# Performance work log

Measured on AMD Instinct MI355X. Metric: run time of the kernel, lower is better.

## Reference

```python
import jax, jax.numpy as jnp
import numpy as np

D_MODEL = 768
NUM_HEADS = 12
D_K = D_MODEL // NUM_HEADS
B, S = 2, 2048


def setup_inputs() -> dict:
    key = jax.random.key(0)
    ks = jax.random.split(key, 7)
    scale = 1.0 / np.sqrt(D_MODEL)
    return {
        "query": jax.random.normal(ks[0], (B, S, D_MODEL), jnp.float32),
        "key_in": jax.random.normal(ks[1], (B, S, D_MODEL), jnp.float32),
        "value": jax.random.normal(ks[2], (B, S, D_MODEL), jnp.float32),
        # nn.Linear weights are [out, in]; y = x @ W.T
        "Wq": jax.random.normal(ks[3], (D_MODEL, D_MODEL), jnp.float32) * scale,
        "Wk": jax.random.normal(ks[4], (D_MODEL, D_MODEL), jnp.float32) * scale,
        "Wv": jax.random.normal(ks[5], (D_MODEL, D_MODEL), jnp.float32) * scale,
        "Wo": jax.random.normal(ks[6], (D_MODEL, D_MODEL), jnp.float32) * scale,
    }


def _split_heads(x):
    b, s, _ = x.shape
    return x.reshape(b, s, NUM_HEADS, D_K).transpose(0, 2, 1, 3)  # [B,H,S,Dk]


def reference(query, key_in, value, Wq, Wk, Wv, Wo):
    Q = _split_heads(query @ Wq.T)
    K = _split_heads(key_in @ Wk.T)
    V = _split_heads(value @ Wv.T)
    scores = jnp.einsum("bhqd,bhkd->bhqk", Q, K) / jnp.sqrt(jnp.float32(D_K))
    attn = jax.nn.softmax(scores, axis=-1)
    ctx = jnp.einsum("bhqk,bhkd->bhqd", attn, V)  # [B,H,S,Dk]
    ctx = ctx.transpose(0, 2, 1, 3).reshape(query.shape[0], query.shape[1], D_MODEL)
    return ctx @ Wo.T
```

## Files before the change

kernel.cpp:

```cpp
#include <hip/hip_runtime.h>
#include <hip/hip_bf16.h>


typedef __bf16 bf16x8 __attribute__((ext_vector_type(8)));
typedef float f32x4 __attribute__((ext_vector_type(4)));
typedef unsigned short u16;
typedef unsigned int u32;
typedef u16 u16x8 __attribute__((ext_vector_type(8)));
typedef u16 u16x4 __attribute__((ext_vector_type(4)));

#define SEQ 2048
#define DM  768
#define NH  12
#define DK  64
#define NBH 24
#define MTOT 4096
#define NEL 3145728
#define NWL 589824

__device__ __forceinline__ u16 f2b(float v) {
  __bf16 t = (__bf16)v;
  return __builtin_bit_cast(u16, t);
}

__device__ __forceinline__ void gl_lds16(const u16* g, u16* l) {
  __builtin_amdgcn_global_load_lds(
      (const __attribute__((address_space(1))) void*)g,
      (__attribute__((address_space(3))) void*)l, 16, 0, 0);
}

__device__ __forceinline__ int pos32(int k) {
  return (k < 16) ? (((k >> 2) << 3) + (k & 3))
                  : ((((k & 15) >> 2) << 3) + (k & 3) + 4);
}


__global__ __launch_bounds__(256) void to_bf16(
    const float* __restrict__ s0, const float* __restrict__ s1, const float* __restrict__ s2,
    const float* __restrict__ s3, const float* __restrict__ s4, const float* __restrict__ s5,
    const float* __restrict__ s6, u16* __restrict__ Xb, u16* __restrict__ Wb)
{
  size_t c = (size_t)blockIdx.x * 256 + threadIdx.x;
  const float* src;
  u16* dst;
  if (c < 1179648) {
    int seg = (int)(c / 393216);
    size_t off = (c % 393216) * 8;
    src = (seg == 0 ? s0 : seg == 1 ? s1 : s2) + off;
    dst = Xb + (size_t)seg * NEL + off;
  } else {
    size_t c2 = c - 1179648;
    int seg = (int)(c2 / 73728);
    size_t off = (c2 % 73728) * 8;
    src = (seg == 0 ? s3 : seg == 1 ? s4 : seg == 2 ? s5 : s6) + off;
    dst = Wb + (size_t)seg * NWL + off;
  }
  float4 f0 = *(const float4*)(src);
  float4 f1 = *(const float4*)(src + 4);
  u16x8 o;
  o[0] = f2b(f0.x); o[1] = f2b(f0.y); o[2] = f2b(f0.z); o[3] = f2b(f0.w);
  o[4] = f2b(f1.x); o[5] = f2b(f1.y); o[6] = f2b(f1.z); o[7] = f2b(f1.w);
  *(u16x8*)dst = o;
}

__device__ __forceinline__ void gemm2_core(
    const u16* __restrict__ X, const u16* __restrict__ W, void* __restrict__ Y,
    int m0, int n0, int mode, u16* As, u16* Bs)
{
  const int tid  = threadIdx.x;
  const int lane = tid & 63, w = tid >> 6;
  const int l15  = lane & 15, quad = lane >> 4;
  const int wm   = (w & 1) * 64, wn = (w >> 1) * 64;

  f32x4 acc[4][4] = {};

  for (int k0 = 0; k0 < DM; k0 += 64) {
    __syncthreads();
#pragma unroll
    for (int i = 0; i < 4; i++) {
      int c = (w * 4 + i) * 64 + lane;
      int row = c >> 3, c8 = c & 7;
      int g8 = c8 ^ (row & 7);
      gl_lds16(X + (size_t)(m0 + row) * DM + k0 + g8 * 8, As + c * 8);
      gl_lds16(W + (size_t)(n0 + row) * DM + k0 + g8 * 8, Bs + c * 8);
    }
    __syncthreads();
#pragma unroll
    for (int dk = 0; dk < 2; dk++) {
      bf16x8 af[4], bf[4];
      int ph = ((dk * 4 + quad) ^ (l15 & 7)) * 8;
#pragma unroll
      for (int t = 0; t < 4; t++) {
        af[t] = *(const bf16x8*)(&As[(wm + t * 16 + l15) * 64 + ph]);
        bf[t] = *(const bf16x8*)(&Bs[(wn + t * 16 + l15) * 64 + ph]);
      }
#pragma unroll
      for (int mt = 0; mt < 4; mt++)
#pragma unroll
        for (int nt = 0; nt < 4; nt++)
          acc[mt][nt] = __builtin_amdgcn_mfma_f32_16x16x32_bf16(af[mt], bf[nt], acc[mt][nt], 0, 0, 0);
    }
  }

  if (mode == 2) {
    float* O = (float*)Y;
#pragma unroll
    for (int mt = 0; mt < 4; mt++) {
      int mg = m0 + wm + mt * 16 + quad * 4;
#pragma unroll
      for (int nt = 0; nt < 4; nt++) {
        int j = n0 + wn + nt * 16 + l15;
#pragma unroll
        for (int r = 0; r < 4; r++)
          O[(size_t)(mg + r) * DM + j] = acc[mt][nt][r];
      }
    }
  } else if (mode == 1) {
    u16* O = (u16*)Y;
#pragma unroll
    for (int mt = 0; mt < 4; mt++) {
      int mg = m0 + wm + mt * 16 + quad * 4;
      int b = mg >> 11, s = mg & 2047;
      int sp = (s & ~31) | pos32(s & 31);
#pragma unroll
      for (int nt = 0; nt < 4; nt++) {
        int j = n0 + wn + nt * 16 + l15;
        int h = j >> 6, d = j & 63;
        u16x4 o;
#pragma unroll
        for (int r = 0; r < 4; r++) o[r] = f2b(acc[mt][nt][r]);
        *(u16x4*)&O[((size_t)(b * NH + h) * DK + d) * SEQ + sp] = o;
      }
    }
  } else {
    u16* O = (u16*)Y;
    u16* T = As;
#pragma unroll
    for (int h2 = 0; h2 < 2; h2++) {
      __syncthreads();
      if ((w & 1) == h2) {
#pragma unroll
        for (int mt = 0; mt < 4; mt++)
#pragma unroll
          for (int nt = 0; nt < 4; nt++)
#pragma unroll
            for (int r = 0; r < 4; r++)
              T[(mt * 16 + quad * 4 + r) * 128 + wn + nt * 16 + l15] = f2b(acc[mt][nt][r]);
      }
      __syncthreads();
#pragma unroll
      for (int i = 0; i < 4; i++) {
        int c = i * 256 + tid;
        int row = c >> 4, ch = c & 15;
        u16x8 val = *(const u16x8*)&T[row * 128 + ch * 8];
        int m = m0 + h2 * 64 + row;
        int j = n0 + ch * 8;
        int hh = j >> 6, d = j & 63;
        int b = m >> 11, s = m & 2047;
        *(u16x8*)&O[((size_t)(b * NH + hh) * SEQ + s) * DK + d] = val;
      }
    }
  }
}

__global__ __launch_bounds__(256) void qkv2(
    const u16* __restrict__ Xb, const u16* __restrict__ Wb,
    u16* __restrict__ Qhm, u16* __restrict__ Khm, u16* __restrict__ Vt)
{
  __shared__ __align__(16) u16 As[128 * 64];
  __shared__ __align__(16) u16 Bs[128 * 64];
  int mat = blockIdx.z;
  const u16* X = Xb + (size_t)mat * NEL;
  const u16* W = Wb + (size_t)mat * NWL;
  void* Y = (mat == 0) ? (void*)Qhm : (mat == 1) ? (void*)Khm : (void*)Vt;
  gemm2_core(X, W, Y, blockIdx.y * 128, blockIdx.x * 128, (mat == 2) ? 1 : 0, As, Bs);
}

__global__ __launch_bounds__(256) void bt2(
    const u16* __restrict__ Ctx, const u16* __restrict__ Wob, float* __restrict__ Y)
{
  __shared__ __align__(16) u16 As[128 * 64];
  __shared__ __align__(16) u16 Bs[128 * 64];
  gemm2_core(Ctx, Wob, Y, blockIdx.y * 128, blockIdx.x * 128, 2, As, Bs);
}

__global__ __launch_bounds__(256) void attn2(
    const u16* __restrict__ Qh, const u16* __restrict__ Kh,
    const u16* __restrict__ Vt, u16* __restrict__ ctx)
{
  __shared__ __align__(16) u16 smem[128 * 64 + 64 * 128];
  __shared__ float Ls[64];
  u16* Ks = smem;
  u16* Vs = smem + 128 * 64;

  const int tid  = threadIdx.x;
  const int lane = tid & 63, w = tid >> 6;
  const int l15  = lane & 15, quad = lane >> 4;
  const int qh = w & 1, kh = w >> 1;
  const int qt = blockIdx.x, bh = blockIdx.y;
  const int b = bh / NH, h = bh % NH;

  const u16* Qb = Qh + (size_t)bh * SEQ * DK;
  const u16* Kb = Kh + (size_t)bh * SEQ * DK;
  const u16* Vb = Vt + (size_t)bh * DK * SEQ;
  const int q0 = qt * 64 + qh * 32;

  bf16x8 qf[2][2];
#pragma unroll
  for (int QT = 0; QT < 2; QT++)
#pragma unroll
    for (int dk = 0; dk < 2; dk++)
      qf[QT][dk] = *(const bf16x8*)&Qb[(size_t)(q0 + QT * 16 + l15) * DK + dk * 32 + quad * 8];

  float lpart[2] = {0.f, 0.f};
  f32x4 oacc[4][2] = {};

  for (int kt = 0; kt < SEQ; kt += 128) {
    __syncthreads();
#pragma unroll
    for (int i = 0; i < 4; i++) {
      int c = (w * 4 + i) * 64 + lane;
      int row = c >> 3, c8 = c & 7;
      gl_lds16(Kb + (size_t)(kt + row) * DK + (c8 ^ (row & 7)) * 8, Ks + c * 8);
    }
#pragma unroll
    for (int i = 0; i < 4; i++) {
      int c = (w * 4 + i) * 64 + lane;
      int d = c >> 4, c16 = c & 15;
      gl_lds16(Vb + (size_t)d * SEQ + kt + (c16 ^ (d & 15)) * 8, Vs + c * 8);
    }
    __syncthreads();

    f32x4 sc[4][2] = {};
#pragma unroll
    for (int MT = 0; MT < 4; MT++) {
      int row = kh * 64 + MT * 16 + l15;
#pragma unroll
      for (int dk = 0; dk < 2; dk++) {
        bf16x8 kf = *(const bf16x8*)&Ks[row * 64 + ((dk * 4 + quad) ^ (l15 & 7)) * 8];
        sc[MT][0] = __builtin_amdgcn_mfma_f32_16x16x32_bf16(kf, qf[0][dk], sc[MT][0], 0, 0, 0);
        sc[MT][1] = __builtin_amdgcn_mfma_f32_16x16x32_bf16(kf, qf[1][dk], sc[MT][1], 0, 0, 0);
      }
    }

    bf16x8 pf[2][2];
#pragma unroll
    for (int QT = 0; QT < 2; QT++)
#pragma unroll
      for (int kk = 0; kk < 2; kk++)
#pragma unroll
        for (int j = 0; j < 8; j++) {
          float s = sc[kk * 2 + (j >> 2)][QT][j & 3] * 0.125f;
          float p = __expf(fminf(s, 30.0f));
          lpart[QT] += p;
          pf[kk][QT][j] = (__bf16)p;
        }

#pragma unroll
    for (int kk = 0; kk < 2; kk++) {
      int cL = kh * 8 + kk * 4 + quad;
#pragma unroll
      for (int DT = 0; DT < 4; DT++) {
        int d = DT * 16 + l15;
        bf16x8 vf = *(const bf16x8*)&Vs[d * 128 + (cL ^ (d & 15)) * 8];
        oacc[DT][0] = __builtin_amdgcn_mfma_f32_16x16x32_bf16(vf, pf[kk][0], oacc[DT][0], 0, 0, 0);
        oacc[DT][1] = __builtin_amdgcn_mfma_f32_16x16x32_bf16(vf, pf[kk][1], oacc[DT][1], 0, 0, 0);
      }
    }
  }

  __syncthreads();

  float lw[2];
#pragma unroll
  for (int QT = 0; QT < 2; QT++) {
    float l = lpart[QT];
    l += __shfl_xor(l, 16);
    l += __shfl_xor(l, 32);
    lw[QT] = l;
  }

  float* Os = (float*)smem;
  float* Ob = Os + qh * (32 * 68);
  if (kh == 1) {
#pragma unroll
    for (int DT = 0; DT < 4; DT++)
#pragma unroll
      for (int QT = 0; QT < 2; QT++)
        *(f32x4*)&Ob[(QT * 16 + l15) * 68 + DT * 16 + quad * 4] = oacc[DT][QT];
    if (quad == 0) {
      Ls[qh * 32 + l15]      = lw[0];
      Ls[qh * 32 + 16 + l15] = lw[1];
    }
  }
  __syncthreads();
  if (kh == 0) {
#pragma unroll
    for (int QT = 0; QT < 2; QT++) {
      float inv = 1.0f / (lw[QT] + Ls[qh * 32 + QT * 16 + l15]);
      int s = q0 + QT * 16 + l15;
#pragma unroll
      for (int DT = 0; DT < 4; DT++) {
        f32x4 add = *(const f32x4*)&Ob[(QT * 16 + l15) * 68 + DT * 16 + quad * 4];
        u16x4 ov;
#pragma unroll
        for (int r = 0; r < 4; r++)
          ov[r] = f2b((oacc[DT][QT][r] + add[r]) * inv);
        *(u16x4*)&ctx[((size_t)(b * SEQ + s)) * DM + h * DK + DT * 16 + quad * 4] = ov;
      }
    }
  }
}


__device__ __forceinline__ void stage8(u16* dst, const void* src, size_t elemIdx, int isf32) {
  if (isf32) {
    const float* s = (const float*)src + elemIdx;
    float4 f0 = *(const float4*)(s);
    float4 f1 = *(const float4*)(s + 4);
    u16x8 o;
    o[0] = f2b(f0.x); o[1] = f2b(f0.y); o[2] = f2b(f0.z); o[3] = f2b(f0.w);
    o[4] = f2b(f1.x); o[5] = f2b(f1.y); o[6] = f2b(f1.z); o[7] = f2b(f1.w);
    *(u16x8*)dst = o;
  } else {
    *(float4*)dst = *(const float4*)((const u16*)src + elemIdx);
  }
}

__device__ __forceinline__ void gemm_core_fb(
    const void* __restrict__ X, const void* __restrict__ W, void* __restrict__ Y,
    int m0, int n0, int out_mode, u16* As, u16* Bs, int xf32, int wf32)
{
  const int tid  = threadIdx.x;
  const int lane = tid & 63, w = tid >> 6;
  const int l15  = lane & 15, quad = lane >> 4;
  const int wm   = (w & 1) * 64, wn = (w >> 1) * 64;
  f32x4 acc[4][4] = {};
  for (int k0 = 0; k0 < DM; k0 += 32) {
    __syncthreads();
#pragma unroll
    for (int i = 0; i < 2; i++) {
      int c = i * 256 + tid;
      int row = c >> 2, cc = c & 3;
      stage8(&As[c * 8], X, (size_t)(m0 + row) * DM + k0 + cc * 8, xf32);
      stage8(&Bs[c * 8], W, (size_t)(n0 + row) * DM + k0 + cc * 8, wf32);
    }
    __syncthreads();
    bf16x8 af[4], bf[4];
#pragma unroll
    for (int t = 0; t < 4; t++) {
      af[t] = *(const bf16x8*)(&As[(wm + t * 16 + l15) * 32 + quad * 8]);
      bf[t] = *(const bf16x8*)(&Bs[(wn + t * 16 + l15) * 32 + quad * 8]);
    }
#pragma unroll
    for (int mt = 0; mt < 4; mt++)
#pragma unroll
      for (int nt = 0; nt < 4; nt++)
        acc[mt][nt] = __builtin_amdgcn_mfma_f32_16x16x32_bf16(af[mt], bf[nt], acc[mt][nt], 0, 0, 0);
  }
  if (out_mode == 2) {
    float* O = (float*)Y;
#pragma unroll
    for (int mt = 0; mt < 4; mt++) {
      int mg = m0 + wm + mt * 16 + quad * 4;
#pragma unroll
      for (int nt = 0; nt < 4; nt++) {
        int j = n0 + wn + nt * 16 + l15;
#pragma unroll
        for (int r = 0; r < 4; r++)
          O[(size_t)(mg + r) * DM + j] = acc[mt][nt][r];
      }
    }
  } else {
    u16* O = (u16*)Y;
#pragma unroll
    for (int mt = 0; mt < 4; mt++) {
      int mg = m0 + wm + mt * 16 + quad * 4;
#pragma unroll
      for (int nt = 0; nt < 4; nt++) {
        int j = n0 + wn + nt * 16 + l15;
        int h = j >> 6, d = j & 63;
#pragma unroll
        for (int r = 0; r < 4; r++) {
          int m = mg + r;
          int b = m >> 11, s = m & 2047;
          O[((size_t)(b * NH + h) * SEQ + s) * DK + d] = f2b(acc[mt][nt][r]);
        }
      }
    }
  }
}

__global__ __launch_bounds__(256) void fb_qkv_gemm(
    const float* __restrict__ Xq, const float* __restrict__ Xk, const float* __restrict__ Xv,
    const float* __restrict__ Wq, const float* __restrict__ Wk, const float* __restrict__ Wv,
    u16* __restrict__ Yq, u16* __restrict__ Yk, u16* __restrict__ Yv)
{
  __shared__ __align__(16) u16 As[128 * 32];
  __shared__ __align__(16) u16 Bs[128 * 32];
  int mat = blockIdx.z;
  const float* X = (mat == 0) ? Xq : (mat == 1) ? Xk : Xv;
  const float* W = (mat == 0) ? Wq : (mat == 1) ? Wk : Wv;
  u16*         Y = (mat == 0) ? Yq : (mat == 1) ? Yk : Yv;
  gemm_core_fb(X, W, Y, blockIdx.y * 128, blockIdx.x * 128, 0, As, Bs, 1, 1);
}

__global__ __launch_bounds__(256) void fb_gemm_bt(
    const u16* __restrict__ X, const float* __restrict__ W, float* __restrict__ Y)
{
  __shared__ __align__(16) u16 As[128 * 32];
  __shared__ __align__(16) u16 Bs[128 * 32];
  gemm_core_fb(X, W, Y, blockIdx.y * 128, blockIdx.x * 128, 2, As, Bs, 0, 1);
}

__global__ __launch_bounds__(256) void fb_attn(
    const u16* __restrict__ Qh, const u16* __restrict__ Kh,
    const u16* __restrict__ Vh, u16* __restrict__ ctx)
{
  __shared__ __align__(16) u16 Ks[32 * 88];
  __shared__ __align__(16) u16 Vs[64 * 40];
  __shared__ __align__(16) u16 Ps[4][16 * 32];
  const int tid  = threadIdx.x;
  const int lane = tid & 63, w = tid >> 6;
  const int l15  = lane & 15, quad = lane >> 4;
  const int qt = blockIdx.x, bh = blockIdx.y;
  const int b = bh / NH, h = bh % NH;
  const u16* Qb = Qh + (size_t)bh * SEQ * DK;
  const u16* Kb = Kh + (size_t)bh * SEQ * DK;
  const u16* Vb = Vh + (size_t)bh * SEQ * DK;
  const int q0 = qt * 64 + w * 16;
  bf16x8 qf[2];
#pragma unroll
  for (int kk = 0; kk < 2; kk++)
    qf[kk] = *(const bf16x8*)(&Qb[(size_t)(q0 + l15) * DK + kk * 32 + quad * 8]);
  float m_i[4] = {-INFINITY, -INFINITY, -INFINITY, -INFINITY};
  float l_i[4] = {0.f, 0.f, 0.f, 0.f};
  f32x4 acc[4] = {};
  for (int kt = 0; kt < SEQ; kt += 32) {
    __syncthreads();
    {
      int c = tid;
      int row = c >> 3, c8 = c & 7;
      *(float4*)(&Ks[row * 88 + c8 * 8]) =
          *(const float4*)(&Kb[(size_t)(kt + row) * DK + c8 * 8]);
    }
#pragma unroll
    for (int i = 0; i < 4; i++) {
      int e = i * 256 + tid;
      int k = e >> 5, d2 = e & 31;
      u32 v = *(const u32*)(&Vb[(size_t)(kt + k) * DK + d2 * 2]);
      Vs[(d2 * 2)     * 40 + k] = (u16)(v & 0xffffu);
      Vs[(d2 * 2 + 1) * 40 + k] = (u16)(v >> 16);
    }
    __syncthreads();
    f32x4 sc[2] = {};
#pragma unroll
    for (int ktt = 0; ktt < 2; ktt++)
#pragma unroll
      for (int dk = 0; dk < 2; dk++) {
        bf16x8 kf = *(const bf16x8*)(&Ks[(ktt * 16 + l15) * 88 + dk * 32 + quad * 8]);
        sc[ktt] = __builtin_amdgcn_mfma_f32_16x16x32_bf16(qf[dk], kf, sc[ktt], 0, 0, 0);
      }
    float alph[4];
#pragma unroll
    for (int r = 0; r < 4; r++) {
      float s0 = sc[0][r] * 0.125f;
      float s1 = sc[1][r] * 0.125f;
      float mv = fmaxf(s0, s1);
      mv = fmaxf(mv, __shfl_xor(mv, 1));
      mv = fmaxf(mv, __shfl_xor(mv, 2));
      mv = fmaxf(mv, __shfl_xor(mv, 4));
      mv = fmaxf(mv, __shfl_xor(mv, 8));
      float mnew = fmaxf(m_i[r], mv);
      float a = __expf(m_i[r] - mnew);
      m_i[r] = mnew;
      float p0 = __expf(s0 - mnew);
      float p1 = __expf(s1 - mnew);
      float rs = p0 + p1;
      rs += __shfl_xor(rs, 1);
      rs += __shfl_xor(rs, 2);
      rs += __shfl_xor(rs, 4);
      rs += __shfl_xor(rs, 8);
      l_i[r] = l_i[r] * a + rs;
      alph[r] = a;
      Ps[w][(quad * 4 + r) * 32 +      l15] = f2b(p0);
      Ps[w][(quad * 4 + r) * 32 + 16 + l15] = f2b(p1);
    }
#pragma unroll
    for (int nt = 0; nt < 4; nt++) {
      acc[nt][0] *= alph[0];
      acc[nt][1] *= alph[1];
      acc[nt][2] *= alph[2];
      acc[nt][3] *= alph[3];
    }
    __syncthreads();
    bf16x8 pf = *(const bf16x8*)(&Ps[w][l15 * 32 + quad * 8]);
#pragma unroll
    for (int nt = 0; nt < 4; nt++) {
      bf16x8 vf = *(const bf16x8*)(&Vs[(nt * 16 + l15) * 40 + quad * 8]);
      acc[nt] = __builtin_amdgcn_mfma_f32_16x16x32_bf16(pf, vf, acc[nt], 0, 0, 0);
    }
  }
#pragma unroll
  for (int nt = 0; nt < 4; nt++) {
    int d = nt * 16 + l15;
#pragma unroll
    for (int r = 0; r < 4; r++) {
      int s = q0 + quad * 4 + r;
      float v = acc[nt][r] / l_i[r];
      ctx[((size_t)(b * SEQ + s)) * DM + h * DK + d] = f2b(v);
    }
  }
}


extern "C" void kernel_launch(void* const* d_in, const int* in_sizes, int n_in,
                              void* d_out, int out_size, void* d_ws, size_t ws_size,
                              hipStream_t stream) {
  const float* act[3] = {nullptr, nullptr, nullptr};
  const float* wgt[4] = {nullptr, nullptr, nullptr, nullptr};
  int na = 0, nw = 0;
  for (int i = 0; i < n_in && i < 7; i++) {
    if (in_sizes[i] == NEL) { if (na < 3) act[na++] = (const float*)d_in[i]; }
    else                    { if (nw < 4) wgt[nw++] = (const float*)d_in[i]; }
  }
  const float* q  = act[0] ? act[0] : (const float*)d_in[0];
  const float* k  = act[1] ? act[1] : (const float*)d_in[1];
  const float* v  = act[2] ? act[2] : (const float*)d_in[2];
  const float* Wq = wgt[0] ? wgt[0] : (const float*)d_in[3];
  const float* Wk = wgt[1] ? wgt[1] : (const float*)d_in[4];
  const float* Wv = wgt[2] ? wgt[2] : (const float*)d_in[5];
  const float* Wo = wgt[3] ? wgt[3] : (const float*)d_in[6];
  u16* ws = (u16*)d_ws;

  const size_t NE = NEL, NW = NWL;
  const size_t need = (6 * NE + 4 * NW) * 2;

  if (ws_size >= need) {
    u16* Xb  = ws;
    u16* Wb  = ws + 3 * NE;
    u16* Qhm = Wb + 4 * NW;
    u16* Khm = Qhm + NE;
    u16* Vt  = Khm + NE;
    u16* Ctx = ws;

    to_bf16<<<5760, 256, 0, stream>>>(q, k, v, Wq, Wk, Wv, Wo, Xb, Wb);
    qkv2<<<dim3(DM / 128, MTOT / 128, 3), 256, 0, stream>>>(Xb, Wb, Qhm, Khm, Vt);
    attn2<<<dim3(SEQ / 64, NBH), 256, 0, stream>>>(Qhm, Khm, Vt, Ctx);
    bt2<<<dim3(DM / 128, MTOT / 128), 256, 0, stream>>>(Ctx, Wb + 3 * NW, (float*)d_out);
  } else {
    u16* Qhm = ws;
    u16* Khm = ws + NE;
    u16* Vhm = ws + 2 * NE;
    u16* Ctx = ws + 3 * NE;
    fb_qkv_gemm<<<dim3(DM / 128, MTOT / 128, 3), 256, 0, stream>>>(
        q, k, v, Wq, Wk, Wv, Qhm, Khm, Vhm);
    fb_attn<<<dim3(SEQ / 64, NBH), 256, 0, stream>>>(Qhm, Khm, Vhm, Ctx);
    fb_gemm_bt<<<dim3(DM / 128, MTOT / 128), 256, 0, stream>>>(Ctx, Wo, (float*)d_out);
  }
}
```

Measured before the change: 194.2 us.

## Double-buffer GEMM and attention tiles, remap blocks per XCD, fold softmax scale

The projection and output GEMMs, and the attention kernel, now double-buffer their LDS tiles so the next global-to-LDS load is issued while the current tile is being computed. Blocks are mapped onto a 1D grid with an XCD-aware ordering, and launch bounds request two blocks per CU. The softmax scale (1/sqrt(d_k) * log2 e) is folded into the Q projection, so attention can use exp2 directly. Row sums are accumulated with an MFMA against a vector of ones, and each wave now covers 32 queries across all keys, which removes the cross-wave LDS reduction at the end. The trade-offs are twice the LDS per block and the loss of the score clamp, which raises overflow risk for large logits.

After: 166.3 us. -14.3%, faster.

```diff
diff --git a/kernel.cpp b/kernel.cpp
--- a/kernel.cpp
+++ b/kernel.cpp
@@ -17,6 +17,9 @@
 #define MTOT 4096
 #define NEL 3145728
 #define NWL 589824
+#define QSCALE 0.18033688f
+
+#define MFMA16 __builtin_amdgcn_mfma_f32_16x16x32_bf16
 
 __device__ __forceinline__ u16 f2b(float v) {
   __bf16 t = (__bf16)v;
@@ -63,9 +66,46 @@
   *(u16x8*)dst = o;
 }
 
+
+__device__ __forceinline__ void g2_stage(
+    const u16* __restrict__ X, const u16* __restrict__ W,
+    int m0, int n0, int k0, u16* As, u16* Bs, int w, int lane)
+{
+#pragma unroll
+  for (int i = 0; i < 4; i++) {
+    int c = (w * 4 + i) * 64 + lane;
+    int row = c >> 3, c8 = c & 7;
+    int g8 = c8 ^ (row & 7);
+    gl_lds16(X + (size_t)(m0 + row) * DM + k0 + g8 * 8, As + c * 8);
+    gl_lds16(W + (size_t)(n0 + row) * DM + k0 + g8 * 8, Bs + c * 8);
+  }
+}
+
+__device__ __forceinline__ void g2_compute(
+    const u16* As, const u16* Bs, f32x4 (&acc)[4][4],
+    int wm, int wn, int l15, int quad)
+{
+#pragma unroll
+  for (int dk = 0; dk < 2; dk++) {
+    bf16x8 af[4], bf[4];
+    int ph = ((dk * 4 + quad) ^ (l15 & 7)) * 8;
+#pragma unroll
+    for (int t = 0; t < 4; t++) {
+      af[t] = *(const bf16x8*)(&As[(wm + t * 16 + l15) * 64 + ph]);
+      bf[t] = *(const bf16x8*)(&Bs[(wn + t * 16 + l15) * 64 + ph]);
+    }
+#pragma unroll
+    for (int mt = 0; mt < 4; mt++)
+#pragma unroll
+      for (int nt = 0; nt < 4; nt++)
+        acc[mt][nt] = MFMA16(af[mt], bf[nt], acc[mt][nt], 0, 0, 0);
+  }
+}
+
 __device__ __forceinline__ void gemm2_core(
     const u16* __restrict__ X, const u16* __restrict__ W, void* __restrict__ Y,
-    int m0, int n0, int mode, u16* As, u16* Bs)
+    int m0, int n0, int mode, float scale,
+    u16* AsA, u16* BsA, u16* AsB, u16* BsB)
 {
   const int tid  = threadIdx.x;
   const int lane = tid & 63, w = tid >> 6;
@@ -74,32 +114,16 @@
 
   f32x4 acc[4][4] = {};
 
-  for (int k0 = 0; k0 < DM; k0 += 64) {
-    __syncthreads();
-#pragma unroll
-    for (int i = 0; i < 4; i++) {
-      int c = (w * 4 + i) * 64 + lane;
-      int row = c >> 3, c8 = c & 7;
-      int g8 = c8 ^ (row & 7);
-      gl_lds16(X + (size_t)(m0 + row) * DM + k0 + g8 * 8, As + c * 8);
-      gl_lds16(W + (size_t)(n0 + row) * DM + k0 + g8 * 8, Bs + c * 8);
-    }
-    __syncthreads();
-#pragma unroll
-    for (int dk = 0; dk < 2; dk++) {
-      bf16x8 af[4], bf[4];
-      int ph = ((dk * 4 + quad) ^ (l15 & 7)) * 8;
-#pragma unroll
-      for (int t = 0; t < 4; t++) {
-        af[t] = *(const bf16x8*)(&As[(wm + t * 16 + l15) * 64 + ph]);
-        bf[t] = *(const bf16x8*)(&Bs[(wn + t * 16 + l15) * 64 + ph]);
-      }
-#pragma unroll
-      for (int mt = 0; mt < 4; mt++)
-#pragma unroll
-        for (int nt = 0; nt < 4; nt++)
-          acc[mt][nt] = __builtin_amdgcn_mfma_f32_16x16x32_bf16(af[mt], bf[nt], acc[mt][nt], 0, 0, 0);
-    }
+  g2_stage(X, W, m0, n0, 0, AsA, BsA, w, lane);
+  __syncthreads();
+#pragma unroll
+  for (int kp = 0; kp < 12; kp += 2) {
+    if (kp + 1 < 12) g2_stage(X, W, m0, n0, (kp + 1) * 64, AsB, BsB, w, lane);
+    g2_compute(AsA, BsA, acc, wm, wn, l15, quad);
+    __syncthreads();
+    if (kp + 2 < 12) g2_stage(X, W, m0, n0, (kp + 2) * 64, AsA, BsA, w, lane);
+    g2_compute(AsB, BsB, acc, wm, wn, l15, quad);
+    __syncthreads();
   }
 
   if (mode == 2) {
@@ -134,7 +158,7 @@
     }
   } else {
     u16* O = (u16*)Y;
-    u16* T = As;
+    u16* T = AsA;
 #pragma unroll
     for (int h2 = 0; h2 < 2; h2++) {
       __syncthreads();
@@ -145,7 +169,7 @@
           for (int nt = 0; nt < 4; nt++)
 #pragma unroll
             for (int r = 0; r < 4; r++)
-              T[(mt * 16 + quad * 4 + r) * 128 + wn + nt * 16 + l15] = f2b(acc[mt][nt][r]);
+              T[(mt * 16 + quad * 4 + r) * 128 + wn + nt * 16 + l15] = f2b(acc[mt][nt][r] * scale);
       }
       __syncthreads();
 #pragma unroll
@@ -163,151 +187,158 @@
   }
 }
 
-__global__ __launch_bounds__(256) void qkv2(
+__global__ __launch_bounds__(256, 2) void qkv2(
     const u16* __restrict__ Xb, const u16* __restrict__ Wb,
     u16* __restrict__ Qhm, u16* __restrict__ Khm, u16* __restrict__ Vt)
 {
-  __shared__ __align__(16) u16 As[128 * 64];
-  __shared__ __align__(16) u16 Bs[128 * 64];
-  int mat = blockIdx.z;
+  __shared__ __align__(16) u16 AsA[128 * 64];
+  __shared__ __align__(16) u16 BsA[128 * 64];
+  __shared__ __align__(16) u16 AsB[128 * 64];
+  __shared__ __align__(16) u16 BsB[128 * 64];
+  int L = blockIdx.x;
+  int xcd = L & 7, i = L >> 3;
+  int m = xcd * 4 + (i & 3);
+  int rest = i >> 2;
+  int n = rest % 6, mat = rest / 6;
   const u16* X = Xb + (size_t)mat * NEL;
   const u16* W = Wb + (size_t)mat * NWL;
   void* Y = (mat == 0) ? (void*)Qhm : (mat == 1) ? (void*)Khm : (void*)Vt;
-  gemm2_core(X, W, Y, blockIdx.y * 128, blockIdx.x * 128, (mat == 2) ? 1 : 0, As, Bs);
-}
-
-__global__ __launch_bounds__(256) void bt2(
+  float scale = (mat == 0) ? QSCALE : 1.0f;
+  gemm2_core(X, W, Y, m * 128, n * 128, (mat == 2) ? 1 : 0, scale, AsA, BsA, AsB, BsB);
+}
+
+__global__ __launch_bounds__(256, 2) void bt2(
     const u16* __restrict__ Ctx, const u16* __restrict__ Wob, float* __restrict__ Y)
 {
-  __shared__ __align__(16) u16 As[128 * 64];
-  __shared__ __align__(16) u16 Bs[128 * 64];
-  gemm2_core(Ctx, Wob, Y, blockIdx.y * 128, blockIdx.x * 128, 2, As, Bs);
-}
-
-__global__ __launch_bounds__(256) void attn2(
+  __shared__ __align__(16) u16 AsA[128 * 64];
+  __shared__ __align__(16) u16 BsA[128 * 64];
+  __shared__ __align__(16) u16 AsB[128 * 64];
+  __shared__ __align__(16) u16 BsB[128 * 64];
+  int L = blockIdx.x;
+  int xcd = L & 7, i = L >> 3;
+  int m = xcd * 4 + (i & 3);
+  int n = i >> 2;
+  gemm2_core(Ctx, Wob, Y, m * 128, n * 128, 2, 1.0f, AsA, BsA, AsB, BsB);
+}
+
+
+__device__ __forceinline__ void attn_stage(
+    const u16* __restrict__ Kb, const u16* __restrict__ Vb, int kt,
+    u16* Ks, u16* Vs, int w, int lane)
+{
+#pragma unroll
+  for (int i = 0; i < 4; i++) {
+    int c = (w * 4 + i) * 64 + lane;
+    int row = c >> 3, c8 = c & 7;
+    gl_lds16(Kb + (size_t)(kt + row) * DK + (c8 ^ (row & 7)) * 8, Ks + c * 8);
+  }
+#pragma unroll
+  for (int i = 0; i < 4; i++) {
+    int c = (w * 4 + i) * 64 + lane;
+    int d = c >> 4, c16 = c & 15;
+    gl_lds16(Vb + (size_t)d * SEQ + kt + (c16 ^ (d & 15)) * 8, Vs + c * 8);
+  }
+}
+
+__device__ __forceinline__ void attn_compute(
+    const u16* Ks, const u16* Vs, const bf16x8 (&qf)[2][2], bf16x8 onef,
+    f32x4 (&oacc)[4][2], f32x4 (&lacc)[2], int l15, int quad)
+{
+#pragma unroll
+  for (int kh2 = 0; kh2 < 2; kh2++) {
+    f32x4 sc[4][2] = {};
+#pragma unroll
+    for (int MT = 0; MT < 4; MT++) {
+      int row = kh2 * 64 + MT * 16 + l15;
+#pragma unroll
+      for (int dk = 0; dk < 2; dk++) {
+        bf16x8 kf = *(const bf16x8*)&Ks[row * 64 + ((dk * 4 + quad) ^ (l15 & 7)) * 8];
+        sc[MT][0] = MFMA16(kf, qf[0][dk], sc[MT][0], 0, 0, 0);
+        sc[MT][1] = MFMA16(kf, qf[1][dk], sc[MT][1], 0, 0, 0);
+      }
+    }
+#pragma unroll
+    for (int g2 = 0; g2 < 2; g2++) {
+      bf16x8 pf[2];
+#pragma unroll
+      for (int QT = 0; QT < 2; QT++) {
+#pragma unroll
+        for (int j = 0; j < 8; j++)
+          pf[QT][j] = (__bf16)__builtin_amdgcn_exp2f(sc[g2 * 2 + (j >> 2)][QT][j & 3]);
+        lacc[QT] = MFMA16(onef, pf[QT], lacc[QT], 0, 0, 0);
+      }
+      int cL = (kh2 * 2 + g2) * 4 + quad;
+#pragma unroll
+      for (int DT = 0; DT < 4; DT++) {
+        int d = DT * 16 + l15;
+        bf16x8 vf = *(const bf16x8*)&Vs[d * 128 + (cL ^ (d & 15)) * 8];
+        oacc[DT][0] = MFMA16(vf, pf[0], oacc[DT][0], 0, 0, 0);
+        oacc[DT][1] = MFMA16(vf, pf[1], oacc[DT][1], 0, 0, 0);
+      }
+    }
+  }
+}
+
+__global__ __launch_bounds__(256, 2) void attn4(
     const u16* __restrict__ Qh, const u16* __restrict__ Kh,
     const u16* __restrict__ Vt, u16* __restrict__ ctx)
 {
-  __shared__ __align__(16) u16 smem[128 * 64 + 64 * 128];
-  __shared__ float Ls[64];
-  u16* Ks = smem;
-  u16* Vs = smem + 128 * 64;
+  __shared__ __align__(16) u16 KsA[128 * 64];
+  __shared__ __align__(16) u16 VsA[64 * 128];
+  __shared__ __align__(16) u16 KsB[128 * 64];
+  __shared__ __align__(16) u16 VsB[64 * 128];
 
   const int tid  = threadIdx.x;
   const int lane = tid & 63, w = tid >> 6;
   const int l15  = lane & 15, quad = lane >> 4;
-  const int qh = w & 1, kh = w >> 1;
-  const int qt = blockIdx.x, bh = blockIdx.y;
+  int L = blockIdx.x;
+  int xcd = L & 7, i = L >> 3;
+  const int bh = xcd * 3 + (i % 3);
+  const int qb = i / 3;
   const int b = bh / NH, h = bh % NH;
 
   const u16* Qb = Qh + (size_t)bh * SEQ * DK;
   const u16* Kb = Kh + (size_t)bh * SEQ * DK;
   const u16* Vb = Vt + (size_t)bh * DK * SEQ;
-  const int q0 = qt * 64 + qh * 32;
+  const int qw = qb * 128 + w * 32;
 
   bf16x8 qf[2][2];
 #pragma unroll
   for (int QT = 0; QT < 2; QT++)
 #pragma unroll
     for (int dk = 0; dk < 2; dk++)
-      qf[QT][dk] = *(const bf16x8*)&Qb[(size_t)(q0 + QT * 16 + l15) * DK + dk * 32 + quad * 8];
-
-  float lpart[2] = {0.f, 0.f};
+      qf[QT][dk] = *(const bf16x8*)&Qb[(size_t)(qw + QT * 16 + l15) * DK + dk * 32 + quad * 8];
+
+  bf16x8 onef;
+#pragma unroll
+  for (int j = 0; j < 8; j++) onef[j] = (__bf16)1.0f;
+
   f32x4 oacc[4][2] = {};
-
-  for (int kt = 0; kt < SEQ; kt += 128) {
-    __syncthreads();
-#pragma unroll
-    for (int i = 0; i < 4; i++) {
-      int c = (w * 4 + i) * 64 + lane;
-      int row = c >> 3, c8 = c & 7;
-      gl_lds16(Kb + (size_t)(kt + row) * DK + (c8 ^ (row & 7)) * 8, Ks + c * 8);
-    }
-#pragma unroll
-    for (int i = 0; i < 4; i++) {
-      int c = (w * 4 + i) * 64 + lane;
-      int d = c >> 4, c16 = c & 15;
-      gl_lds16(Vb + (size_t)d * SEQ + kt + (c16 ^ (d & 15)) * 8, Vs + c * 8);
-    }
-    __syncthreads();
-
-    f32x4 sc[4][2] = {};
-#pragma unroll
-    for (int MT = 0; MT < 4; MT++) {
-      int row = kh * 64 + MT * 16 + l15;
-#pragma unroll
-      for (int dk = 0; dk < 2; dk++) {
-        bf16x8 kf = *(const bf16x8*)&Ks[row * 64 + ((dk * 4 + quad) ^ (l15 & 7)) * 8];
-        sc[MT][0] = __builtin_amdgcn_mfma_f32_16x16x32_bf16(kf, qf[0][dk], sc[MT][0], 0, 0, 0);
-        sc[MT][1] = __builtin_amdgcn_mfma_f32_16x16x32_bf16(kf, qf[1][dk], sc[MT][1], 0, 0, 0);
-      }
-    }
-
-    bf16x8 pf[2][2];
-#pragma unroll
-    for (int QT = 0; QT < 2; QT++)
-#pragma unroll
-      for (int kk = 0; kk < 2; kk++)
-#pragma unroll
-        for (int j = 0; j < 8; j++) {
-          float s = sc[kk * 2 + (j >> 2)][QT][j & 3] * 0.125f;
-          float p = __expf(fminf(s, 30.0f));
-          lpart[QT] += p;
-          pf[kk][QT][j] = (__bf16)p;
-        }
-
-#pragma unroll
-    for (int kk = 0; kk < 2; kk++) {
-      int cL = kh * 8 + kk * 4 + quad;
-#pragma unroll
-      for (int DT = 0; DT < 4; DT++) {
-        int d = DT * 16 + l15;
-        bf16x8 vf = *(const bf16x8*)&Vs[d * 128 + (cL ^ (d & 15)) * 8];
-        oacc[DT][0] = __builtin_amdgcn_mfma_f32_16x16x32_bf16(vf, pf[kk][0], oacc[DT][0], 0, 0, 0);
-        oacc[DT][1] = __builtin_amdgcn_mfma_f32_16x16x32_bf16(vf, pf[kk][1], oacc[DT][1], 0, 0, 0);
-      }
-    }
-  }
-
+  f32x4 lacc[2] = {};
+
+  attn_stage(Kb, Vb, 0, KsA, VsA, w, lane);
   __syncthreads();
-
-  float lw[2];
+#pragma unroll
+  for (int kp = 0; kp < 16; kp += 2) {
+    if (kp + 1 < 16) attn_stage(Kb, Vb, (kp + 1) * 128, KsB, VsB, w, lane);
+    attn_compute(KsA, VsA, qf, onef, oacc, lacc, l15, quad);
+    __syncthreads();
+    if (kp + 2 < 16) attn_stage(Kb, Vb, (kp + 2) * 128, KsA, VsA, w, lane);
+    attn_compute(KsB, VsB, qf, onef, oacc, lacc, l15, quad);
+    __syncthreads();
+  }
+
 #pragma unroll
   for (int QT = 0; QT < 2; QT++) {
-    float l = lpart[QT];
-    l += __shfl_xor(l, 16);
-    l += __shfl_xor(l, 32);
-    lw[QT] = l;
-  }
-
-  float* Os = (float*)smem;
-  float* Ob = Os + qh * (32 * 68);
-  if (kh == 1) {
-#pragma unroll
-    for (int DT = 0; DT < 4; DT++)
-#pragma unroll
-      for (int QT = 0; QT < 2; QT++)
-        *(f32x4*)&Ob[(QT * 16 + l15) * 68 + DT * 16 + quad * 4] = oacc[DT][QT];
-    if (quad == 0) {
-      Ls[qh * 32 + l15]      = lw[0];
-      Ls[qh * 32 + 16 + l15] = lw[1];
-    }
-  }
-  __syncthreads();
-  if (kh == 0) {
-#pragma unroll
-    for (int QT = 0; QT < 2; QT++) {
-      float inv = 1.0f / (lw[QT] + Ls[qh * 32 + QT * 16 + l15]);
-      int s = q0 + QT * 16 + l15;
-#pragma unroll
-      for (int DT = 0; DT < 4; DT++) {
-        f32x4 add = *(const f32x4*)&Ob[(QT * 16 + l15) * 68 + DT * 16 + quad * 4];
-        u16x4 ov;
-#pragma unroll
-        for (int r = 0; r < 4; r++)
-          ov[r] = f2b((oacc[DT][QT][r] + add[r]) * inv);
-        *(u16x4*)&ctx[((size_t)(b * SEQ + s)) * DM + h * DK + DT * 16 + quad * 4] = ov;
-      }
+    int q = qw + QT * 16 + l15;
+    float inv = 1.0f / lacc[QT][0];
+#pragma unroll
+    for (int DT = 0; DT < 4; DT++) {
+      u16x4 ov;
+#pragma unroll
+      for (int r = 0; r < 4; r++)
+        ov[r] = f2b(oacc[DT][QT][r] * inv);
+      *(u16x4*)&ctx[((size_t)(b * SEQ + q)) * DM + h * DK + DT * 16 + quad * 4] = ov;
     }
   }
 }
@@ -356,7 +387,7 @@
     for (int mt = 0; mt < 4; mt++)
 #pragma unroll
       for (int nt = 0; nt < 4; nt++)
-        acc[mt][nt] = __builtin_amdgcn_mfma_f32_16x16x32_bf16(af[mt], bf[nt], acc[mt][nt], 0, 0, 0);
+        acc[mt][nt] = MFMA16(af[mt], bf[nt], acc[mt][nt], 0, 0, 0);
   }
   if (out_mode == 2) {
     float* O = (float*)Y;
@@ -459,7 +490,7 @@
 #pragma unroll
       for (int dk = 0; dk < 2; dk++) {
         bf16x8 kf = *(const bf16x8*)(&Ks[(ktt * 16 + l15) * 88 + dk * 32 + quad * 8]);
-        sc[ktt] = __builtin_amdgcn_mfma_f32_16x16x32_bf16(qf[dk], kf, sc[ktt], 0, 0, 0);
+        sc[ktt] = MFMA16(qf[dk], kf, sc[ktt], 0, 0, 0);
       }
     float alph[4];
 #pragma unroll
@@ -498,7 +529,7 @@
 #pragma unroll
     for (int nt = 0; nt < 4; nt++) {
       bf16x8 vf = *(const bf16x8*)(&Vs[(nt * 16 + l15) * 40 + quad * 8]);
-      acc[nt] = __builtin_amdgcn_mfma_f32_16x16x32_bf16(pf, vf, acc[nt], 0, 0, 0);
+      acc[nt] = MFMA16(pf, vf, acc[nt], 0, 0, 0);
     }
   }
 #pragma unroll
@@ -545,9 +576,9 @@
     u16* Ctx = ws;
 
     to_bf16<<<5760, 256, 0, stream>>>(q, k, v, Wq, Wk, Wv, Wo, Xb, Wb);
-    qkv2<<<dim3(DM / 128, MTOT / 128, 3), 256, 0, stream>>>(Xb, Wb, Qhm, Khm, Vt);
-    attn2<<<dim3(SEQ / 64, NBH), 256, 0, stream>>>(Qhm, Khm, Vt, Ctx);
-    bt2<<<dim3(DM / 128, MTOT / 128), 256, 0, stream>>>(Ctx, Wb + 3 * NW, (float*)d_out);
+    qkv2<<<576, 256, 0, stream>>>(Xb, Wb, Qhm, Khm, Vt);
+    attn4<<<384, 256, 0, stream>>>(Qhm, Khm, Vt, Ctx);
+    bt2<<<192, 256, 0, stream>>>(Ctx, Wb + 3 * NW, (float*)d_out);
   } else {
     u16* Qhm = ws;
     u16* Khm = ws + NE;
```
